# Kernel optimization log

Measured on AMD Instinct MI355X. Metric: run time of the kernel, lower is better.

The kernel has to match this reference:

```python
import jax, jax.numpy as jnp
import numpy as np

# Static skeleton structure (mirrors init_kwargs adj_list)
J = 25            # joints (second dim of x)
E = 24            # edges, sorted keys 0..23
DEG = 2           # neighbors per edge: adj[i] = [i, i+1]
P = E * DEG       # total (edge, neighbor) conv pairs = 48
CIN, COUT, K = 16, 16, 3
L = 65536
LOUT = L - K + 1  # VALID conv, stride 1 (torch Conv1d defaults)

# pair p = (edge p//DEG, neighbor index below) in edge-sorted order
PAIR_NBR = np.array([j for i in range(E) for j in (i, i + 1)], dtype=np.int32)  # (P,)


def setup_inputs() -> dict:
    key = jax.random.key(0)
    k1, k2, k3 = jax.random.split(key, 3)
    x = jax.random.normal(k1, (CIN, J, L), dtype=jnp.float32)
    # per-(edge,neighbor) Conv1d weights/biases, stacked in edge-sorted pair order
    W = jax.random.normal(k2, (P, COUT, CIN, K), dtype=jnp.float32) * 0.05
    b = jax.random.normal(k3, (P, COUT), dtype=jnp.float32) * 0.05
    return {"x": x, "W": W, "b": b}


def reference(x, W, b):
    # gather neighbor slices for every (edge, neighbor) pair: (CIN, P, L) -> (P, CIN, L)
    nbr = jnp.asarray(PAIR_NBR)
    xg = jnp.transpose(x[:, nbr, :], (1, 0, 2))
    # one grouped conv replaces P tiny Conv1d launches: groups = P
    lhs = xg.reshape(1, P * CIN, L)
    rhs = W.reshape(P * COUT, CIN, K)
    out = jax.lax.conv_general_dilated(
        lhs, rhs, window_strides=(1,), padding='VALID',
        feature_group_count=P, dimension_numbers=('NCH', 'OIH', 'NCH'))
    out = out.reshape(P, COUT, LOUT) + b[:, :, None]   # (P, COUT, LOUT)
    # average over each edge's neighbors (uniform degree DEG)
    y = out.reshape(E, DEG, COUT, LOUT).mean(axis=1)   # (E, COUT, LOUT)
    # torch stacks per-edge (COUT, LOUT) results at dim=1 -> (COUT, E, LOUT)
    return jnp.transpose(y, (1, 0, 2))
```

## Files before the change

### kernel.cpp

```cpp
#include <hip/hip_runtime.h>
#include <hip/hip_bf16.h>


#define NJ    25
#define LSEQ  65536
#define NE    24
#define LOUTN (LSEQ - 2)
#define NWA   (NE * 3 * 64 * 4)
#define NBR   (NE * 16)
#define CW    260

typedef __attribute__((ext_vector_type(8))) short bf16x8;
typedef __attribute__((ext_vector_type(4))) float f32x4;

static __device__ __forceinline__ unsigned short f2bf(float f) {
    unsigned u = __float_as_uint(f);
    u += 0x7FFFu + ((u >> 16) & 1u);
    return (unsigned short)(u >> 16);
}

static __device__ __forceinline__ unsigned cvtpk(float lo, float hi) {
    union { __hip_bfloat162 h; unsigned u; } cv;
    cv.h = __float22bfloat162_rn(make_float2(lo, hi));
    return cv.u;
}

__global__ void repack_kernel(const float* __restrict__ W, const float* __restrict__ b,
                              unsigned* __restrict__ Wa, float* __restrict__ Br)
{
    int idx = blockIdx.x * 256 + threadIdx.x;
    if (idx < NWA) {
        int d = idx & 3;
        int l = (idx >> 2) & 63;
        int k = (idx >> 8) % 3;
        int e = (idx >> 8) / 3;
        int g = l >> 4, co = l & 15;
        unsigned packed = 0;
        #pragma unroll
        for (int h = 0; h < 2; ++h) {
            int i  = 2 * d + h;
            int kk = 8 * g + i;
            int ci = kk >> 1, j = kk & 1;
            float w = 0.5f * W[(((2 * e + j) * 16 + co) * 16 + ci) * 3 + k];
            packed |= (unsigned)f2bf(w) << (16 * h);
        }
        Wa[idx] = packed;
    }
    if (idx < NBR) {
        int e = idx >> 4, co = idx & 15;
        Br[idx] = 0.5f * (b[(2 * e) * 16 + co] + b[(2 * e + 1) * 16 + co]);
    }
}

__global__ __launch_bounds__(256)
void skel_mfma_kernel(const float* __restrict__ x,
                      const unsigned* __restrict__ Wa,
                      const float* __restrict__ Br,
                      float* __restrict__ out)
{
    __shared__ unsigned lds[16 * CW];

    const int e   = blockIdx.y;
    const int tb  = blockIdx.x * 256;
    const int tid = threadIdx.x;
    const int l   = tid & 63, wv = tid >> 6;
    const int g   = l >> 4,  lc = l & 15;

    {
        const int rp = tid >> 4;
        const int q0 = tid & 15;
        const float* xlo = x + (size_t)(rp * NJ + e) * LSEQ + tb;
        #pragma unroll
        for (int s = 0; s < 4; ++s) {
            const int c = 4 * q0 + 64 * s;
            float4 lo = *reinterpret_cast<const float4*>(xlo + c);
            float4 hi = *reinterpret_cast<const float4*>(xlo + LSEQ + c);
            uint4 pk;
            pk.x = cvtpk(lo.x, hi.x);
            pk.y = cvtpk(lo.y, hi.y);
            pk.z = cvtpk(lo.z, hi.z);
            pk.w = cvtpk(lo.w, hi.w);
            *reinterpret_cast<uint4*>(&lds[rp * CW + c]) = pk;
        }
    }
    if (tid < 32) {
        const int rp = tid >> 1, h = tid & 1;
        const int gc = min(tb + 256 + h, LSEQ - 1);
        const float* xl = x + (size_t)(rp * NJ + e) * LSEQ;
        lds[rp * CW + 256 + h] = cvtpk(xl[gc], xl[gc + LSEQ]);
    }
    __syncthreads();

    union { uint4 q; bf16x8 v; } A[3];
    #pragma unroll
    for (int k = 0; k < 3; ++k)
        A[k].q = *reinterpret_cast<const uint4*>(Wa + ((e * 3 + k) * 64 + l) * 4);

    const float4 bias = *reinterpret_cast<const float4*>(Br + e * 16 + g * 4);

    #pragma unroll
    for (int tc = 0; tc < 4; ++tc) {
        const int cb = wv * 64 + tc * 16 + lc;
        f32x4 C;
        C[0] = bias.x; C[1] = bias.y; C[2] = bias.z; C[3] = bias.w;
        #pragma unroll
        for (int k = 0; k < 3; ++k) {
            union { unsigned u[4]; bf16x8 v8; } B;
            #pragma unroll
            for (int d = 0; d < 4; ++d)
                B.u[d] = lds[(4 * g + d) * CW + cb + k];
            C = __builtin_amdgcn_mfma_f32_16x16x32_bf16(A[k].v, B.v8, C, 0, 0, 0);
        }
        const int t = tb + cb;
        if (t < LOUTN) {
            #pragma unroll
            for (int r = 0; r < 4; ++r)
                out[(size_t)((g * 4 + r) * NE + e) * LOUTN + t] = C[r];
        }
    }
}

extern "C" void kernel_launch(void* const* d_in, const int* in_sizes, int n_in,
                              void* d_out, int out_size, void* d_ws, size_t ws_size,
                              hipStream_t stream)
{
    const float* x = (const float*)d_in[0];
    const float* W = (const float*)d_in[1];
    const float* b = (const float*)d_in[2];
    float* out     = (float*)d_out;

    unsigned* Wa = (unsigned*)d_ws;
    float*    Br = (float*)(Wa + NWA);

    repack_kernel<<<(NWA + 255) / 256, 256, 0, stream>>>(W, b, Wa, Br);

    dim3 grid((LOUTN + 255) / 256, NE);
    skel_mfma_kernel<<<grid, 256, 0, stream>>>(x, Wa, Br, out);
}
```

Before: 46.22 us.

## Fuse weight repack into conv kernel and swap MFMA operands for vector stores

Drops the separate repack kernel launch: each thread now loads fp32 weights straight from W, converts them to bf16, and computes the averaged bias itself. The MFMA operands are swapped so that x becomes the A operand and the weights the B operand. Each lane's accumulators then hold four consecutive time steps, so the output can be written as float2 vector stores instead of scalar strided stores. The 0.5 averaging factor is applied in the epilogue. This trades one extra launch for redundant per-block weight loads and conversions.

```diff
diff --git a/kernel.cpp b/kernel.cpp
--- a/kernel.cpp
+++ b/kernel.cpp
@@ -6,18 +6,10 @@
 #define LSEQ  65536
 #define NE    24
 #define LOUTN (LSEQ - 2)
-#define NWA   (NE * 3 * 64 * 4)
-#define NBR   (NE * 16)
 #define CW    260
 
 typedef __attribute__((ext_vector_type(8))) short bf16x8;
 typedef __attribute__((ext_vector_type(4))) float f32x4;
-
-static __device__ __forceinline__ unsigned short f2bf(float f) {
-    unsigned u = __float_as_uint(f);
-    u += 0x7FFFu + ((u >> 16) & 1u);
-    return (unsigned short)(u >> 16);
-}
 
 static __device__ __forceinline__ unsigned cvtpk(float lo, float hi) {
     union { __hip_bfloat162 h; unsigned u; } cv;
@@ -25,37 +17,10 @@
     return cv.u;
 }
 
-__global__ void repack_kernel(const float* __restrict__ W, const float* __restrict__ b,
-                              unsigned* __restrict__ Wa, float* __restrict__ Br)
-{
-    int idx = blockIdx.x * 256 + threadIdx.x;
-    if (idx < NWA) {
-        int d = idx & 3;
-        int l = (idx >> 2) & 63;
-        int k = (idx >> 8) % 3;
-        int e = (idx >> 8) / 3;
-        int g = l >> 4, co = l & 15;
-        unsigned packed = 0;
-        #pragma unroll
-        for (int h = 0; h < 2; ++h) {
-            int i  = 2 * d + h;
-            int kk = 8 * g + i;
-            int ci = kk >> 1, j = kk & 1;
-            float w = 0.5f * W[(((2 * e + j) * 16 + co) * 16 + ci) * 3 + k];
-            packed |= (unsigned)f2bf(w) << (16 * h);
-        }
-        Wa[idx] = packed;
-    }
-    if (idx < NBR) {
-        int e = idx >> 4, co = idx & 15;
-        Br[idx] = 0.5f * (b[(2 * e) * 16 + co] + b[(2 * e + 1) * 16 + co]);
-    }
-}
-
 __global__ __launch_bounds__(256)
 void skel_mfma_kernel(const float* __restrict__ x,
-                      const unsigned* __restrict__ Wa,
-                      const float* __restrict__ Br,
+                      const float* __restrict__ W,
+                      const float* __restrict__ b,
                       float* __restrict__ out)
 {
     __shared__ unsigned lds[16 * CW];
@@ -65,6 +30,23 @@
     const int tid = threadIdx.x;
     const int l   = tid & 63, wv = tid >> 6;
     const int g   = l >> 4,  lc = l & 15;
+
+    const float* wp = W + ((size_t)((2 * e) * 16 + lc) * 16 + 4 * g) * 3;
+    f32x4 wj0[3], wj1[3];
+    #pragma unroll
+    for (int q = 0; q < 3; ++q) {
+        wj0[q] = *reinterpret_cast<const f32x4*>(wp + 4 * q);
+        wj1[q] = *reinterpret_cast<const f32x4*>(wp + 768 + 4 * q);
+    }
+    union { unsigned u[4]; bf16x8 v8; } Bw[3];
+    #pragma unroll
+    for (int d = 0; d < 4; ++d)
+        #pragma unroll
+        for (int k = 0; k < 3; ++k) {
+            const int f = d * 3 + k;
+            Bw[k].u[d] = cvtpk(wj0[f >> 2][f & 3], wj1[f >> 2][f & 3]);
+        }
+    const float bhalf = 0.5f * (b[(2 * e) * 16 + lc] + b[(2 * e + 1) * 16 + lc]);
 
     {
         const int rp = tid >> 4;
@@ -91,31 +73,33 @@
     }
     __syncthreads();
 
-    union { uint4 q; bf16x8 v; } A[3];
-    #pragma unroll
-    for (int k = 0; k < 3; ++k)
-        A[k].q = *reinterpret_cast<const uint4*>(Wa + ((e * 3 + k) * 64 + l) * 4);
-
-    const float4 bias = *reinterpret_cast<const float4*>(Br + e * 16 + g * 4);
-
     #pragma unroll
     for (int tc = 0; tc < 4; ++tc) {
-        const int cb = wv * 64 + tc * 16 + lc;
-        f32x4 C;
-        C[0] = bias.x; C[1] = bias.y; C[2] = bias.z; C[3] = bias.w;
+        const int tt0 = wv * 64 + tc * 16;
+        f32x4 C = {0.f, 0.f, 0.f, 0.f};
         #pragma unroll
         for (int k = 0; k < 3; ++k) {
-            union { unsigned u[4]; bf16x8 v8; } B;
+            union { unsigned u[4]; bf16x8 v8; } Ax;
             #pragma unroll
             for (int d = 0; d < 4; ++d)
-                B.u[d] = lds[(4 * g + d) * CW + cb + k];
-            C = __builtin_amdgcn_mfma_f32_16x16x32_bf16(A[k].v, B.v8, C, 0, 0, 0);
+                Ax.u[d] = lds[(4 * g + d) * CW + tt0 + lc + k];
+            C = __builtin_amdgcn_mfma_f32_16x16x32_bf16(Ax.v8, Bw[k].v8, C, 0, 0, 0);
         }
-        const int t = tb + cb;
-        if (t < LOUTN) {
-            #pragma unroll
-            for (int r = 0; r < 4; ++r)
-                out[(size_t)((g * 4 + r) * NE + e) * LOUTN + t] = C[r];
+
+        const int t0p = tb + tt0 + 4 * g;
+        float* op = out + (size_t)(lc * NE + e) * LOUTN + t0p;
+        float v0 = fmaf(0.5f, C[0], bhalf);
+        float v1 = fmaf(0.5f, C[1], bhalf);
+        float v2 = fmaf(0.5f, C[2], bhalf);
+        float v3 = fmaf(0.5f, C[3], bhalf);
+        if (t0p + 3 < LOUTN) {
+            *reinterpret_cast<float2*>(op)     = make_float2(v0, v1);
+            *reinterpret_cast<float2*>(op + 2) = make_float2(v2, v3);
+        } else {
+            if (t0p     < LOUTN) op[0] = v0;
+            if (t0p + 1 < LOUTN) op[1] = v1;
+            if (t0p + 2 < LOUTN) op[2] = v2;
+            if (t0p + 3 < LOUTN) op[3] = v3;
         }
     }
 }
@@ -129,11 +113,6 @@
     const float* b = (const float*)d_in[2];
     float* out     = (float*)d_out;
 
-    unsigned* Wa = (unsigned*)d_ws;
-    float*    Br = (float*)(Wa + NWA);
-
-    repack_kernel<<<(NWA + 255) / 256, 256, 0, stream>>>(W, b, Wa, Br);
-
     dim3 grid((LOUTN + 255) / 256, NE);
-    skel_mfma_kernel<<<grid, 256, 0, stream>>>(x, Wa, Br, out);
+    skel_mfma_kernel<<<grid, 256, 0, stream>>>(x, W, b, out);
 }
```

Measured after the change: 53.27 us. 15.3% more time.
